# Kernel optimization log

Measured on AMD Instinct MI355X. Metric: run time of the kernel, lower is better.

The kernel has to match this reference:

```python
import jax, jax.numpy as jnp
import numpy as np

N_LEVELS = 16
N_FEATS = 2
TABLE_SIZE = 1 << 19          # log2_hashmap_size = 19
BASE_RES = 32
PER_LEVEL_SCALE = 1.3819
RES = 512
CLAMP = 25.133
PRIME_Y = np.uint32(2654435761)
N_PTS = 1 << 19


def hashgrid_encode(table, uv):
    """Instant-NGP style multires hashgrid. table: [L, T, F], uv: [N, 2] in [0,1].
    Returns [N, L*F]."""
    L, T, F = table.shape
    levels = jnp.arange(L)
    res = jnp.floor(BASE_RES * (PER_LEVEL_SCALE ** levels.astype(jnp.float32))).astype(jnp.int32)  # [L]
    # 4 bilinear corner offsets
    offs = jnp.array([[0, 0], [1, 0], [0, 1], [1, 1]], dtype=jnp.int32)  # [4, 2]

    def level_fn(tab_l, res_l):
        pos = uv * res_l.astype(uv.dtype)                       # [N, 2]
        p0 = jnp.clip(jnp.floor(pos).astype(jnp.int32), 0, res_l - 1)
        frac = pos - p0.astype(uv.dtype)                        # [N, 2]
        corners = p0[:, None, :] + offs[None, :, :]             # [N, 4, 2]
        cx = corners[..., 0].astype(jnp.uint32)
        cy = corners[..., 1].astype(jnp.uint32)
        stride = (res_l + 1).astype(jnp.uint32)
        dense_idx = cx + cy * stride                            # dense grid index
        hash_idx = (cx ^ (cy * PRIME_Y)) & jnp.uint32(T - 1)    # spatial hash (T is pow2)
        use_dense = (res_l + 1).astype(jnp.int64) * (res_l + 1).astype(jnp.int64) <= T
        idx = jnp.where(use_dense, dense_idx, hash_idx).astype(jnp.int32)  # [N, 4]
        feats = tab_l[idx]                                      # [N, 4, F] gather
        wx, wy = frac[:, 0], frac[:, 1]
        w = jnp.stack([(1 - wx) * (1 - wy), wx * (1 - wy),
                       (1 - wx) * wy, wx * wy], axis=-1)        # [N, 4]
        return jnp.einsum('ncf,nc->nf', feats, w)               # [N, F]

    out = jax.vmap(level_fn)(table, res)                        # [L, N, F]
    return out.transpose(1, 0, 2).reshape(uv.shape[0], L * F)


def sin_layer(x, W, b):
    h = jnp.clip(x @ W.T + b, -CLAMP, CLAMP)
    return jnp.sin(h)


def setup_inputs() -> dict:
    key = jax.random.key(0)
    ks = jax.random.split(key, 8)
    y = jax.random.randint(ks[0], (N_PTS,), 0, RES, dtype=jnp.int32)
    x = jax.random.randint(ks[1], (N_PTS,), 0, RES, dtype=jnp.int32)
    cam_feat = jax.random.normal(ks[2], (32,), dtype=jnp.float32)
    # NGP tables initialized uniform in [-1e-4, 1e-4]
    table = jax.random.uniform(ks[3], (N_LEVELS, TABLE_SIZE, N_FEATS),
                               minval=-1e-4, maxval=1e-4, dtype=jnp.float32)
    def siren_w(k, outp, inp):
        return jax.random.uniform(k, (outp, inp), minval=-1.0 / inp, maxval=1.0 / inp,
                                  dtype=jnp.float32)
    W1 = siren_w(ks[4], 512, 64)
    W2 = siren_w(ks[5], 512, 512)
    W3 = siren_w(ks[6], 384, 512)
    return {"y": y, "x": x, "cam_feat": cam_feat, "table": table,
            "W1": W1, "b1": jnp.zeros((512,), jnp.float32),
            "W2": W2, "b2": jnp.zeros((512,), jnp.float32),
            "W3": W3, "b3": jnp.zeros((384,), jnp.float32)}


def reference(y, x, cam_feat, table, W1, b1, W2, b2, W3, b3):
    denom = jnp.float32(RES - 1)
    uv = jnp.stack([jnp.clip(x.astype(jnp.float32), 0, RES - 1) / denom,
                    jnp.clip(y.astype(jnp.float32), 0, RES - 1) / denom], axis=-1)  # [N, 2]
    codes = hashgrid_encode(table, uv)                          # [N, 32]
    cam = jnp.broadcast_to(cam_feat[None, :], (codes.shape[0], cam_feat.shape[0]))
    h = jnp.concatenate([codes, cam], axis=-1)                  # [N, 64]
    h = sin_layer(h, W1, b1)
    h = sin_layer(h, W2, b2)
    return sin_layer(h, W3, b3)                                 # [N, 384]
```

## Files before the change

kernel.cpp:

```cpp
#include <hip/hip_runtime.h>

typedef _Float16 half8 __attribute__((ext_vector_type(8)));
typedef _Float16 half4 __attribute__((ext_vector_type(4)));
typedef _Float16 half2v __attribute__((ext_vector_type(2)));
typedef float f32x4 __attribute__((ext_vector_type(4)));

#define TSIZE (1 << 19)
#define TMASK (TSIZE - 1)
#define NT 8

__constant__ int c_res[16] = {32, 44, 61, 84, 116, 161, 222, 307,
                              425, 588, 812, 1123, 1551, 2144, 2963, 4095};

__global__ void hg_cvt_all(const float* __restrict__ W1, const float* __restrict__ W2,
                           const float* __restrict__ W3, _Float16* __restrict__ d) {
  int g = blockIdx.x * blockDim.x + threadIdx.x;
  int i = g * 4;
  const float* s;
  if (i < 32768) s = W1 + i;
  else if (i < 32768 + 262144) s = W2 + (i - 32768);
  else s = W3 + (i - 32768 - 262144);
  float4 v = *(const float4*)s;
  half4 h = {(_Float16)v.x, (_Float16)v.y, (_Float16)v.z, (_Float16)v.w};
  *(half4*)(d + i) = h;
}

__device__ __forceinline__ float sin_act_precise(float x) {
  if (__builtin_expect(fabsf(x) > 1.0f, 0))
    return sinf(fminf(fmaxf(x, -25.133f), 25.133f));
  float x2 = x * x;
  float p = 2.75573192e-6f;
  p = fmaf(p, x2, -1.98412698e-4f);
  p = fmaf(p, x2, 8.33333333e-3f);
  p = fmaf(p, x2, -1.66666667e-1f);
  return fmaf(p * x2, x, x);
}

__device__ __forceinline__ float sin_act_fast(float x) {
  return __sinf(__builtin_amdgcn_fmed3f(x, -25.133f, 25.133f));
}

#define XROW 144
#define SROW 1040
#define SB0 9216
#define SB1 75776
#define LD_X(m, k) (*(const half8*)(&smem[(m) * XROW + (k) * 2]))
#define LD_S(base, m, k) (*(const half8*)(&smem[(base) + (m) * SROW + (k) * 2]))
#define ST_S8(base, m, n, v) \
  do { *(half4*)(&smem[(base) + (m) * SROW + (n) * 2]) = (v); } while (0)

#define MFMA16 __builtin_amdgcn_mfma_f32_16x16x32_f16

__global__ void __launch_bounds__(512, 2)
hg_fused(const int* __restrict__ ybuf, const int* __restrict__ xbuf,
         const float* __restrict__ cam, const float* __restrict__ table,
         const _Float16* __restrict__ W1h, const float* __restrict__ b1,
         const _Float16* __restrict__ W2h, const float* __restrict__ b2,
         const _Float16* __restrict__ W3h, const float* __restrict__ b3,
         float* __restrict__ out) {
  __shared__ __align__(16) unsigned char smem[142336];
  const int t = threadIdx.x;
  const int lane = t & 63;
  const int wid = t >> 6;
  const int l15 = lane & 15;
  const int lhi = lane >> 4;
  const int blk0 = blockIdx.x << 9;
  const f32x4 vzero = {0.f, 0.f, 0.f, 0.f};

  auto ENC = [&](int tile) {
    const int sub = t & 15;
    const int res = c_res[sub];
    const float rf = (float)res;
    const unsigned strd = (unsigned)(res + 1);
    const bool dense = (res <= 723);
    const float* tb = table + ((size_t)sub * TSIZE) * 2;
    const float2 cf = ((const float2*)cam)[sub];
    const half2v hc = {(_Float16)cf.x, (_Float16)cf.y};
    const int pb = blk0 + (tile << 6);
#pragma unroll
    for (int hh = 0; hh < 2; ++hh) {
      const int m = (t >> 4) + hh * 32;
      const int p = pb + m;
      const float u = (float)xbuf[p] / 511.0f;
      const float v = (float)ybuf[p] / 511.0f;
      const float px = u * rf, py = v * rf;
      int p0x = (int)floorf(px); p0x = p0x < 0 ? 0 : (p0x > res - 1 ? res - 1 : p0x);
      int p0y = (int)floorf(py); p0y = p0y < 0 ? 0 : (p0y > res - 1 ? res - 1 : p0y);
      const float fx = px - (float)p0x, fy = py - (float)p0y;
      const float w00 = (1.f - fx) * (1.f - fy), w10 = fx * (1.f - fy);
      const float w01 = (1.f - fx) * fy, w11 = fx * fy;
      float c0 = 0.f, c1 = 0.f;
#pragma unroll
      for (int c = 0; c < 4; ++c) {
        const unsigned cx = (unsigned)(p0x + (c & 1));
        const unsigned cy = (unsigned)(p0y + (c >> 1));
        const unsigned idx = dense ? (cx + cy * strd)
                                   : ((cx ^ (cy * 2654435761u)) & TMASK);
        const float2 f = *(const float2*)(tb + (size_t)idx * 2);
        const float w = (c == 0) ? w00 : (c == 1) ? w10 : (c == 2) ? w01 : w11;
        c0 = fmaf(w, f.x, c0);
        c1 = fmaf(w, f.y, c1);
      }
      half2v hf = {(_Float16)c0, (_Float16)c1};
      *(half2v*)(&smem[m * XROW + 4 * sub]) = hf;
      *(half2v*)(&smem[m * XROW + 64 + 4 * sub]) = hc;
    }
  };

  auto L1F = [&](int sb) {
    const int n0 = wid << 6;
    f32x4 acc[4][4];
#pragma unroll
    for (int i = 0; i < 4; ++i)
#pragma unroll
      for (int j = 0; j < 4; ++j) acc[i][j] = vzero;
#pragma unroll
    for (int ks = 0; ks < 2; ++ks) {
      const int kk = ks * 32 + lhi * 8;
      half8 bw[4];
#pragma unroll
      for (int nf = 0; nf < 4; ++nf)
        bw[nf] = *(const half8*)(W1h + (n0 + nf * 16 + l15) * 64 + kk);
      half8 ax[4];
#pragma unroll
      for (int mf = 0; mf < 4; ++mf) ax[mf] = LD_X(mf * 16 + l15, kk);
#pragma unroll
      for (int mf = 0; mf < 4; ++mf)
#pragma unroll
        for (int nf = 0; nf < 4; ++nf)
          acc[mf][nf] = MFMA16(bw[nf], ax[mf], acc[mf][nf], 0, 0, 0);
    }
#pragma unroll
    for (int nf = 0; nf < 4; ++nf) {
      const int nb = n0 + nf * 16 + lhi * 4;
      const f32x4 bb = *(const f32x4*)(b1 + nb);
#pragma unroll
      for (int mf = 0; mf < 4; ++mf) {
        half4 pk;
#pragma unroll
        for (int r = 0; r < 4; ++r)
          pk[r] = (_Float16)sin_act_fast(acc[mf][nf][r] + bb[r]);
        ST_S8(sb, mf * 16 + l15, nb, pk);
      }
    }
  };

  ENC(0);
  __syncthreads();
  L1F(SB0);
  __syncthreads();

  for (int tt = 0; tt < NT; ++tt) {
    const int sb = (tt & 1) ? SB1 : SB0;
    const int sbn = (tt & 1) ? SB0 : SB1;
    const int n0 = wid << 6;

    f32x4 acc2[4][4];
#pragma unroll
    for (int i = 0; i < 4; ++i)
#pragma unroll
      for (int j = 0; j < 4; ++j) acc2[i][j] = vzero;
    if (tt + 1 < NT) ENC(tt + 1);
#pragma unroll 2
    for (int ks = 0; ks < 16; ++ks) {
      const int kk = ks * 32 + lhi * 8;
      half8 bw[4];
#pragma unroll
      for (int nf = 0; nf < 4; ++nf)
        bw[nf] = *(const half8*)(W2h + (n0 + nf * 16 + l15) * 512 + kk);
      half8 ax[4];
#pragma unroll
      for (int mf = 0; mf < 4; ++mf) ax[mf] = LD_S(sb, mf * 16 + l15, kk);
#pragma unroll
      for (int mf = 0; mf < 4; ++mf)
#pragma unroll
        for (int nf = 0; nf < 4; ++nf)
          acc2[mf][nf] = MFMA16(bw[nf], ax[mf], acc2[mf][nf], 0, 0, 0);
    }
#pragma unroll
    for (int nf = 0; nf < 4; ++nf) {
      const f32x4 bb = *(const f32x4*)(b2 + (n0 + nf * 16 + lhi * 4));
#pragma unroll
      for (int mf = 0; mf < 4; ++mf)
#pragma unroll
        for (int r = 0; r < 4; ++r)
          acc2[mf][nf][r] = sin_act_fast(acc2[mf][nf][r] + bb[r]);
    }
    __syncthreads();

#pragma unroll
    for (int nf = 0; nf < 4; ++nf) {
      const int nb = n0 + nf * 16 + lhi * 4;
#pragma unroll
      for (int mf = 0; mf < 4; ++mf) {
        half4 pk = {(_Float16)acc2[mf][nf][0], (_Float16)acc2[mf][nf][1],
                    (_Float16)acc2[mf][nf][2], (_Float16)acc2[mf][nf][3]};
        ST_S8(sb, mf * 16 + l15, nb, pk);
      }
    }
    __syncthreads();

    if (tt + 1 < NT) L1F(sbn);
    {
      const int c0n = wid * 48;
      f32x4 acc3[4][3];
#pragma unroll
      for (int i = 0; i < 4; ++i)
#pragma unroll
        for (int j = 0; j < 3; ++j) acc3[i][j] = vzero;
#pragma unroll 2
      for (int ks = 0; ks < 16; ++ks) {
        const int kk = ks * 32 + lhi * 8;
        half8 bw[3];
#pragma unroll
        for (int nf = 0; nf < 3; ++nf)
          bw[nf] = *(const half8*)(W3h + (c0n + nf * 16 + l15) * 512 + kk);
        half8 ax[4];
#pragma unroll
        for (int mf = 0; mf < 4; ++mf) ax[mf] = LD_S(sb, mf * 16 + l15, kk);
#pragma unroll
        for (int mf = 0; mf < 4; ++mf)
#pragma unroll
          for (int nf = 0; nf < 3; ++nf)
            acc3[mf][nf] = MFMA16(bw[nf], ax[mf], acc3[mf][nf], 0, 0, 0);
      }
      const int pb = blk0 + (tt << 6);
#pragma unroll
      for (int nf = 0; nf < 3; ++nf) {
        const int nb = c0n + nf * 16 + lhi * 4;
        const f32x4 bb = *(const f32x4*)(b3 + nb);
#pragma unroll
        for (int mf = 0; mf < 4; ++mf) {
          float4 o;
          float* op = &o.x;
#pragma unroll
          for (int r = 0; r < 4; ++r)
            op[r] = sin_act_precise(acc3[mf][nf][r] + bb[r]);
          *(float4*)(out + (size_t)(pb + mf * 16 + l15) * 384 + nb) = o;
        }
      }
    }
    __syncthreads();
  }
}

extern "C" void kernel_launch(void* const* d_in, const int* in_sizes, int n_in,
                              void* d_out, int out_size, void* d_ws, size_t ws_size,
                              hipStream_t stream) {
  const int* y = (const int*)d_in[0];
  const int* x = (const int*)d_in[1];
  const float* cam = (const float*)d_in[2];
  const float* table = (const float*)d_in[3];
  const float* W1 = (const float*)d_in[4];
  const float* b1 = (const float*)d_in[5];
  const float* W2 = (const float*)d_in[6];
  const float* b2 = (const float*)d_in[7];
  const float* W3 = (const float*)d_in[8];
  const float* b3 = (const float*)d_in[9];
  float* out = (float*)d_out;

  _Float16* Wh = (_Float16*)d_ws;
  _Float16* W1h = Wh;
  _Float16* W2h = W1h + 512 * 64;
  _Float16* W3h = W2h + 512 * 512;

  hg_cvt_all<<<480, 256, 0, stream>>>(W1, W2, W3, Wh);

  const int nblocks = (1 << 19) / 512;
  hg_fused<<<nblocks, 512, 0, stream>>>(y, x, cam, table, W1h, b1, W2h, b2, W3h, b3, out);
}
```

Before: 1.301 ms.

## Split block into two ping-pong thread groups alternating encode and MLP tiles

The block grows to 1024 threads, split into two 512-thread groups, each with its own input and activation LDS buffers. The groups stagger their phases so that one group's hash-grid gather and layer-1 work runs while the other group runs the large layer-2 or layer-3 MFMA loops. The goal is to hide gather latency and SFU work behind matrix work without changing the math. In exchange, LDS use rises to about 148 KB and twice as many waves share each CU's register file. That raises the risk of register spills for the 64-register accumulators, and the barrier count per tile pair grows.

```diff
diff --git a/kernel.cpp b/kernel.cpp
--- a/kernel.cpp
+++ b/kernel.cpp
@@ -7,7 +7,7 @@
 
 #define TSIZE (1 << 19)
 #define TMASK (TSIZE - 1)
-#define NT 8
+#define NPAIR 4
 
 __constant__ int c_res[16] = {32, 44, 61, 84, 116, 161, 222, 307,
                               425, 588, 812, 1123, 1551, 2144, 2963, 4095};
@@ -42,33 +42,39 @@
 
 #define XROW 144
 #define SROW 1040
-#define SB0 9216
-#define SB1 75776
-#define LD_X(m, k) (*(const half8*)(&smem[(m) * XROW + (k) * 2]))
-#define LD_S(base, m, k) (*(const half8*)(&smem[(base) + (m) * SROW + (k) * 2]))
-#define ST_S8(base, m, n, v) \
-  do { *(half4*)(&smem[(base) + (m) * SROW + (n) * 2]) = (v); } while (0)
+#define XA_OFF 0
+#define SA_OFF 9216
+#define XB_OFF 75776
+#define SB_OFF 84992
+#define LD_X(xb, m, k) (*(const half8*)(&smem[(xb) + (m) * XROW + (k) * 2]))
+#define LD_S(sb, m, k) (*(const half8*)(&smem[(sb) + (m) * SROW + (k) * 2]))
+#define ST_S8(sb, m, n, v) \
+  do { *(half4*)(&smem[(sb) + (m) * SROW + (n) * 2]) = (v); } while (0)
 
 #define MFMA16 __builtin_amdgcn_mfma_f32_16x16x32_f16
 
-__global__ void __launch_bounds__(512, 2)
+__global__ void __launch_bounds__(1024, 4)
 hg_fused(const int* __restrict__ ybuf, const int* __restrict__ xbuf,
          const float* __restrict__ cam, const float* __restrict__ table,
          const _Float16* __restrict__ W1h, const float* __restrict__ b1,
          const _Float16* __restrict__ W2h, const float* __restrict__ b2,
          const _Float16* __restrict__ W3h, const float* __restrict__ b3,
          float* __restrict__ out) {
-  __shared__ __align__(16) unsigned char smem[142336];
+  __shared__ __align__(16) unsigned char smem[151552];
   const int t = threadIdx.x;
-  const int lane = t & 63;
-  const int wid = t >> 6;
+  const bool gA = (t < 512);
+  const int tl = t & 511;
+  const int lane = tl & 63;
+  const int wid = tl >> 6;
   const int l15 = lane & 15;
   const int lhi = lane >> 4;
+  const int xb = gA ? XA_OFF : XB_OFF;
+  const int sb = gA ? SA_OFF : SB_OFF;
   const int blk0 = blockIdx.x << 9;
   const f32x4 vzero = {0.f, 0.f, 0.f, 0.f};
 
   auto ENC = [&](int tile) {
-    const int sub = t & 15;
+    const int sub = tl & 15;
     const int res = c_res[sub];
     const float rf = (float)res;
     const unsigned strd = (unsigned)(res + 1);
@@ -79,7 +85,7 @@
     const int pb = blk0 + (tile << 6);
 #pragma unroll
     for (int hh = 0; hh < 2; ++hh) {
-      const int m = (t >> 4) + hh * 32;
+      const int m = (tl >> 4) + hh * 32;
       const int p = pb + m;
       const float u = (float)xbuf[p] / 511.0f;
       const float v = (float)ybuf[p] / 511.0f;
@@ -102,12 +108,12 @@
         c1 = fmaf(w, f.y, c1);
       }
       half2v hf = {(_Float16)c0, (_Float16)c1};
-      *(half2v*)(&smem[m * XROW + 4 * sub]) = hf;
-      *(half2v*)(&smem[m * XROW + 64 + 4 * sub]) = hc;
-    }
-  };
-
-  auto L1F = [&](int sb) {
+      *(half2v*)(&smem[xb + m * XROW + 4 * sub]) = hf;
+      *(half2v*)(&smem[xb + m * XROW + 64 + 4 * sub]) = hc;
+    }
+  };
+
+  auto L1F = [&]() {
     const int n0 = wid << 6;
     f32x4 acc[4][4];
 #pragma unroll
@@ -123,7 +129,7 @@
         bw[nf] = *(const half8*)(W1h + (n0 + nf * 16 + l15) * 64 + kk);
       half8 ax[4];
 #pragma unroll
-      for (int mf = 0; mf < 4; ++mf) ax[mf] = LD_X(mf * 16 + l15, kk);
+      for (int mf = 0; mf < 4; ++mf) ax[mf] = LD_X(xb, mf * 16 + l15, kk);
 #pragma unroll
       for (int mf = 0; mf < 4; ++mf)
 #pragma unroll
@@ -145,22 +151,12 @@
     }
   };
 
-  ENC(0);
-  __syncthreads();
-  L1F(SB0);
-  __syncthreads();
-
-  for (int tt = 0; tt < NT; ++tt) {
-    const int sb = (tt & 1) ? SB1 : SB0;
-    const int sbn = (tt & 1) ? SB0 : SB1;
+  auto L2K = [&](f32x4 (&acc2)[4][4]) {
     const int n0 = wid << 6;
-
-    f32x4 acc2[4][4];
 #pragma unroll
     for (int i = 0; i < 4; ++i)
 #pragma unroll
       for (int j = 0; j < 4; ++j) acc2[i][j] = vzero;
-    if (tt + 1 < NT) ENC(tt + 1);
 #pragma unroll 2
     for (int ks = 0; ks < 16; ++ks) {
       const int kk = ks * 32 + lhi * 8;
@@ -186,8 +182,10 @@
         for (int r = 0; r < 4; ++r)
           acc2[mf][nf][r] = sin_act_fast(acc2[mf][nf][r] + bb[r]);
     }
-    __syncthreads();
-
+  };
+
+  auto L2S = [&](f32x4 (&acc2)[4][4]) {
+    const int n0 = wid << 6;
 #pragma unroll
     for (int nf = 0; nf < 4; ++nf) {
       const int nb = n0 + nf * 16 + lhi * 4;
@@ -198,48 +196,67 @@
         ST_S8(sb, mf * 16 + l15, nb, pk);
       }
     }
-    __syncthreads();
-
-    if (tt + 1 < NT) L1F(sbn);
-    {
-      const int c0n = wid * 48;
-      f32x4 acc3[4][3];
-#pragma unroll
-      for (int i = 0; i < 4; ++i)
-#pragma unroll
-        for (int j = 0; j < 3; ++j) acc3[i][j] = vzero;
+  };
+
+  auto L3OUT = [&](int tile) {
+    const int n0 = wid * 48;
+    f32x4 acc3[4][3];
+#pragma unroll
+    for (int i = 0; i < 4; ++i)
+#pragma unroll
+      for (int j = 0; j < 3; ++j) acc3[i][j] = vzero;
 #pragma unroll 2
-      for (int ks = 0; ks < 16; ++ks) {
-        const int kk = ks * 32 + lhi * 8;
-        half8 bw[3];
+    for (int ks = 0; ks < 16; ++ks) {
+      const int kk = ks * 32 + lhi * 8;
+      half8 bw[3];
+#pragma unroll
+      for (int nf = 0; nf < 3; ++nf)
+        bw[nf] = *(const half8*)(W3h + (n0 + nf * 16 + l15) * 512 + kk);
+      half8 ax[4];
+#pragma unroll
+      for (int mf = 0; mf < 4; ++mf) ax[mf] = LD_S(sb, mf * 16 + l15, kk);
+#pragma unroll
+      for (int mf = 0; mf < 4; ++mf)
 #pragma unroll
         for (int nf = 0; nf < 3; ++nf)
-          bw[nf] = *(const half8*)(W3h + (c0n + nf * 16 + l15) * 512 + kk);
-        half8 ax[4];
-#pragma unroll
-        for (int mf = 0; mf < 4; ++mf) ax[mf] = LD_S(sb, mf * 16 + l15, kk);
-#pragma unroll
-        for (int mf = 0; mf < 4; ++mf)
-#pragma unroll
-          for (int nf = 0; nf < 3; ++nf)
-            acc3[mf][nf] = MFMA16(bw[nf], ax[mf], acc3[mf][nf], 0, 0, 0);
-      }
-      const int pb = blk0 + (tt << 6);
-#pragma unroll
-      for (int nf = 0; nf < 3; ++nf) {
-        const int nb = c0n + nf * 16 + lhi * 4;
-        const f32x4 bb = *(const f32x4*)(b3 + nb);
-#pragma unroll
-        for (int mf = 0; mf < 4; ++mf) {
-          float4 o;
-          float* op = &o.x;
-#pragma unroll
-          for (int r = 0; r < 4; ++r)
-            op[r] = sin_act_precise(acc3[mf][nf][r] + bb[r]);
-          *(float4*)(out + (size_t)(pb + mf * 16 + l15) * 384 + nb) = o;
-        }
-      }
-    }
+          acc3[mf][nf] = MFMA16(bw[nf], ax[mf], acc3[mf][nf], 0, 0, 0);
+    }
+    const int pb = blk0 + (tile << 6);
+#pragma unroll
+    for (int nf = 0; nf < 3; ++nf) {
+      const int nb = n0 + nf * 16 + lhi * 4;
+      const f32x4 bb = *(const f32x4*)(b3 + nb);
+#pragma unroll
+      for (int mf = 0; mf < 4; ++mf) {
+        float4 o;
+        float* op = &o.x;
+#pragma unroll
+        for (int r = 0; r < 4; ++r)
+          op[r] = sin_act_precise(acc3[mf][nf][r] + bb[r]);
+        *(float4*)(out + (size_t)(pb + mf * 16 + l15) * 384 + nb) = o;
+      }
+    }
+  };
+
+  if (gA) ENC(0);
+  __syncthreads();
+  if (gA) L1F(); else ENC(1);
+  __syncthreads();
+
+  f32x4 acc2[4][4];
+  for (int k = 0; k < NPAIR; ++k) {
+    if (gA) L2K(acc2); else L1F();
+    __syncthreads();
+    if (gA) L2S(acc2);
+    else if (k < NPAIR - 1) ENC(2 * k + 3);
+    __syncthreads();
+    if (gA) L3OUT(2 * k); else L2K(acc2);
+    __syncthreads();
+    if (gA) { if (k < NPAIR - 1) ENC(2 * k + 2); }
+    else L2S(acc2);
+    __syncthreads();
+    if (gA) { if (k < NPAIR - 1) L1F(); }
+    else L3OUT(2 * k + 1);
     __syncthreads();
   }
 }
@@ -267,5 +284,5 @@
   hg_cvt_all<<<480, 256, 0, stream>>>(W1, W2, W3, Wh);
 
   const int nblocks = (1 << 19) / 512;
-  hg_fused<<<nblocks, 512, 0, stream>>>(y, x, cam, table, W1h, b1, W2h, b2, W3h, b3, out);
-}
+  hg_fused<<<nblocks, 1024, 0, stream>>>(y, x, cam, table, W1h, b1, W2h, b2, W3h, b3, out);
+}
```

Measured after the change: 1.908 ms. 46.7% more time.
